# Performance work log

Hardware: AMD Instinct MI355X
Metric: run time of the kernel (lower is better)

## Reference

```python
import jax, jax.numpy as jnp
import numpy as np

N_NODES = 100000
N_EDGES = 1600000
D_IN, D_HID, N_CLS, N_LAYERS = 128, 256, 10, 3


def setup_inputs() -> dict:
    key = jax.random.key(0)
    ks = jax.random.split(key, 8)
    x = jax.random.normal(ks[0], (N_NODES, D_IN), dtype=jnp.float32)
    edge_index = jax.random.randint(ks[1], (2, N_EDGES), 0, N_NODES, dtype=jnp.int64)
    s = 0.05
    Wl = jax.random.normal(ks[2], (N_LAYERS, D_HID, D_IN), dtype=jnp.float32) * s
    Wr = jax.random.normal(ks[3], (N_LAYERS, D_HID, D_IN), dtype=jnp.float32) * s
    bias = jnp.zeros((N_LAYERS, D_HID), dtype=jnp.float32)
    W1 = jax.random.normal(ks[4], (D_HID, D_HID), dtype=jnp.float32) * s
    b1 = jnp.zeros((D_HID,), dtype=jnp.float32)
    W2 = jax.random.normal(ks[5], (N_CLS, D_HID), dtype=jnp.float32) * s
    b2 = jnp.zeros((N_CLS,), dtype=jnp.float32)
    return {"x": x, "edge_index": edge_index, "Wl": Wl, "Wr": Wr, "bias": bias,
            "W1": W1, "b1": b1, "W2": W2, "b2": b2}


def reference(x, edge_index, Wl, Wr, bias, W1, b1, W2, b2):
    n = x.shape[0]
    src, tgt = edge_index[0], edge_index[1]
    # mean aggregation of source-node features onto targets (SAGEConv aggr='mean')
    deg = jax.ops.segment_sum(jnp.ones(src.shape[0], x.dtype), tgt, num_segments=n)
    agg = jax.ops.segment_sum(x[src], tgt, num_segments=n)  # [N, D_in]
    agg = agg / jnp.clip(deg, 1.0)[:, None]
    # Every layer consumes the ORIGINAL x (per the source forward), so agg is shared.
    h = None
    for l in range(Wl.shape[0]):
        h = jax.nn.relu(agg @ Wl[l].T + x @ Wr[l].T + bias[l])  # [N, D_hid]
    # global_mean_pool over all nodes (single graph)
    pooled = jnp.mean(h, axis=0, keepdims=True)  # [1, D_hid]
    z = jax.nn.relu(pooled @ W1.T + b1)
    z = z @ W2.T + b2
    return jax.nn.log_softmax(z, axis=1)
```

## Files before the change

kernel.cpp:

```cpp
#include <hip/hip_runtime.h>
#include <hip/hip_bf16.h>

#define D_IN  128
#define D_HID 256
#define CBITS 9
#define CSIZE 512
#define EPB   8192
#define CCAP  10240
#define GT_CAP 2048

typedef __bf16 bf16x8 __attribute__((ext_vector_type(8)));
typedef float  f32x4  __attribute__((ext_vector_type(4)));
typedef float  f32x2  __attribute__((ext_vector_type(2)));

__device__ __forceinline__ unsigned short f2bf(float f) {
    unsigned u = __float_as_uint(f);
    u += 0x7FFFu + ((u >> 16) & 1u);
    return (unsigned short)(u >> 16);
}
__device__ __forceinline__ uint2 pack4(float4 v) {
    unsigned lo = (unsigned)f2bf(v.x) | ((unsigned)f2bf(v.y) << 16);
    unsigned hi = (unsigned)f2bf(v.z) | ((unsigned)f2bf(v.w) << 16);
    return make_uint2(lo, hi);
}
__device__ __forceinline__ unsigned packfp8(float4 v) {
    int u = __builtin_amdgcn_cvt_pk_fp8_f32(v.x, v.y, 0, false);
    u = __builtin_amdgcn_cvt_pk_fp8_f32(v.z, v.w, u, true);
    return (unsigned)u;
}
__device__ __forceinline__ void g2lds16(const void* g, void* l) {
    __builtin_amdgcn_global_load_lds(
        (const __attribute__((address_space(1))) unsigned int*)g,
        (__attribute__((address_space(3))) unsigned int*)l, 16, 0, 0);
}

__global__ __launch_bounds__(256)
void prep(const float* __restrict__ x, unsigned short* __restrict__ xb,
          unsigned char* __restrict__ x8,
          const float* __restrict__ Wr2, const float* __restrict__ Wl2,
          unsigned short* __restrict__ Bsw,
          int* __restrict__ gcur, float* __restrict__ pooled_pad,
          long n16, int NXB, int NCB) {
    const int bid = blockIdx.x;
    const int tid = threadIdx.x;
    if (bid < NXB) {
        const long t = (long)bid * 256 + tid;
        if (t >= n16) return;
        const float4* x4 = (const float4*)x;
        float4 v0 = x4[t * 4], v1 = x4[t * 4 + 1], v2 = x4[t * 4 + 2], v3 = x4[t * 4 + 3];
        uint2 p0 = pack4(v0), p1 = pack4(v1), p2 = pack4(v2), p3 = pack4(v3);
        ((uint4*)xb)[t * 2]     = make_uint4(p0.x, p0.y, p1.x, p1.y);
        ((uint4*)xb)[t * 2 + 1] = make_uint4(p2.x, p2.y, p3.x, p3.y);
        ((uint4*)x8)[t] = make_uint4(packfp8(v0), packfp8(v1), packfp8(v2), packfp8(v3));
    } else if (bid < NXB + 32) {
        const int t_idx = (bid - NXB) * 256 + tid;
        const int lane = t_idx & 63;
        const int rest = t_idx >> 6;
        const int tt   = rest & 3;
        const int wn2  = (rest >> 2) & 3;
        const int kk   = rest >> 4;
        const int j = wn2 * 64 + tt * 16 + (lane & 15);
        const int k = kk * 32 + (lane >> 4) * 8;
        const float* src = (k < 128) ? &Wr2[j * 128 + k] : &Wl2[j * 128 + (k - 128)];
        float4 v0 = *(const float4*)src;
        float4 v1 = *(const float4*)(src + 4);
        uint2 p0 = pack4(v0), p1 = pack4(v1);
        *(uint4*)&Bsw[(long)t_idx * 8] = make_uint4(p0.x, p0.y, p1.x, p1.y);
    } else {
        for (int i = tid; i < NCB * 16; i += 256) gcur[i] = 0;
        for (int i = tid; i < 256 * 16; i += 256) pooled_pad[i] = 0.f;
    }
}

__global__ __launch_bounds__(256)
void coarse_bin(const void* __restrict__ ei, int* __restrict__ gcur,
                unsigned* __restrict__ segc, int E, int NCB) {
    __shared__ int cnt[256];
    __shared__ int basel[256];
    __shared__ int s_is64;
    const int tid = threadIdx.x;
    const long e0 = (long)blockIdx.x * EPB;
    const int ecnt = (int)min((long)EPB, (long)E - e0);

    if (tid < 64) {
        const int v = ((const int*)ei)[2 * tid + 1];
        const unsigned long long b = __ballot(v != 0);
        if (tid == 0) s_is64 = (b == 0ull);
    }
    for (int i = tid; i < NCB; i += 256) cnt[i] = 0;
    __syncthreads();
    const int is64 = s_is64;

    for (int j = tid; j < ecnt; j += 256) {
        int t = is64 ? (int)((const long long*)ei)[E + e0 + j]
                     : ((const int*)ei)[E + e0 + j];
        atomicAdd(&cnt[t >> CBITS], 1);
    }
    __syncthreads();

    for (int c = tid; c < NCB; c += 256) {
        const int n = cnt[c];
        const int na = (n + 15) & ~15;
        int b = 0;
        if (na > 0) b = atomicAdd(&gcur[c * 16], na);
        basel[c] = b;
        cnt[c] = 0;
        unsigned* sp = segc + (long)c * CCAP;
        for (int i = n; i < na; ++i)
            if (b + i < CCAP) sp[b + i] = 0xFFFFFFFFu;
    }
    __syncthreads();

    for (int j = tid; j < ecnt; j += 256) {
        int s, t;
        if (is64) { const long long* p = (const long long*)ei; s = (int)p[e0 + j]; t = (int)p[E + e0 + j]; }
        else      { const int* p = (const int*)ei;             s = p[e0 + j];      t = p[E + e0 + j]; }
        const int c = t >> CBITS;
        const int r = atomicAdd(&cnt[c], 1);
        const int pos = basel[c] + r;
        if (pos < CCAP)
            segc[(long)c * CCAP + pos] = ((unsigned)s << CBITS) | (unsigned)(t & (CSIZE - 1));
    }
}

__global__ __launch_bounds__(1024)
void refine(const int* __restrict__ gcur, const unsigned* __restrict__ segc,
            unsigned* __restrict__ gorder, int2* __restrict__ rowdeg, int M) {
    __shared__ unsigned order[CCAP];
    __shared__ int degh[CSIZE], scn[CSIZE], cur[CSIZE];
    const int tid = threadIdx.x;
    const int cb = blockIdx.x;
    const int nbase = cb << CBITS;
    const int nn = min(CSIZE, M - nbase);
    const int len = min(gcur[cb * 16], CCAP);
    const unsigned* sp = segc + (long)cb * CCAP;

    if (tid < CSIZE) degh[tid] = 0;
    __syncthreads();
    for (int i = tid; i < len; i += 1024) {
        const unsigned e = sp[i];
        if (e != 0xFFFFFFFFu) atomicAdd(&degh[e & (CSIZE - 1)], 1);
    }
    __syncthreads();
    if (tid < CSIZE) scn[tid] = degh[tid];
    __syncthreads();
    for (int off = 1; off < CSIZE; off <<= 1) {
        int v = 0;
        if (tid >= off && tid < CSIZE) v = scn[tid - off];
        __syncthreads();
        if (tid < CSIZE) scn[tid] += v;
        __syncthreads();
    }
    if (tid < CSIZE) cur[tid] = scn[tid] - degh[tid];
    __syncthreads();
    for (int i = tid; i < len; i += 1024) {
        const unsigned e = sp[i];
        if (e != 0xFFFFFFFFu) {
            const int r = atomicAdd(&cur[e & (CSIZE - 1)], 1);
            order[r] = (e >> CBITS) << 7;
        }
    }
    __syncthreads();
    const int total = scn[CSIZE - 1];
    unsigned* gp = gorder + (long)cb * CCAP;
    for (int i = tid; i < total; i += 1024) gp[i] = order[i];
    if (tid < nn)
        rowdeg[nbase + tid] = make_int2(cb * CCAP + (scn[tid] - degh[tid]), degh[tid]);
}

__global__ __launch_bounds__(512)
void gather_tile(const unsigned char* __restrict__ x8, const unsigned* __restrict__ gorder,
                 const int2* __restrict__ rowdeg, unsigned short* __restrict__ aggb, int M) {
    __shared__ unsigned ordl[GT_CAP];
    __shared__ int s_start, s_total;
    const int tid = threadIdx.x;
    const int first = blockIdx.x * 64;
    const int nn = min(64, M - first);

    if (tid == 0) {
        int2 r0 = rowdeg[first];
        int2 rl = rowdeg[first + nn - 1];
        s_start = r0.x;
        s_total = min(rl.x + rl.y - r0.x, GT_CAP);
    }
    __syncthreads();
    const int st = s_start, tot = s_total;
    for (int i = tid; i < tot; i += 512) ordl[i] = gorder[st + i];
    __syncthreads();

    const int wave = tid >> 6;
    const int lane = tid & 63;
    const int c2   = lane & 15;
    const int sub  = lane >> 4;
    const unsigned cb = (unsigned)c2 * 8;

    for (int nl = wave; nl < nn; nl += 8) {
        const int node = first + nl;
        const int2 rd = rowdeg[node];
        const int beg = rd.x - st;
        const int deg = min(rd.y, tot - beg);
        f32x2 a0 = {0.f, 0.f}, a1 = {0.f, 0.f}, a2 = {0.f, 0.f}, a3 = {0.f, 0.f};
        int i = 0;
        const int nf = deg & ~7;
        for (; i < nf; i += 8) {
            uint2 v0 = *(const uint2*)(x8 + (ordl[beg + i + sub] + cb));
            uint2 v1 = *(const uint2*)(x8 + (ordl[beg + i + 4 + sub] + cb));
            a0 += __builtin_amdgcn_cvt_pk_f32_fp8(v0.x, false);
            a1 += __builtin_amdgcn_cvt_pk_f32_fp8(v0.x, true);
            a2 += __builtin_amdgcn_cvt_pk_f32_fp8(v0.y, false);
            a3 += __builtin_amdgcn_cvt_pk_f32_fp8(v0.y, true);
            a0 += __builtin_amdgcn_cvt_pk_f32_fp8(v1.x, false);
            a1 += __builtin_amdgcn_cvt_pk_f32_fp8(v1.x, true);
            a2 += __builtin_amdgcn_cvt_pk_f32_fp8(v1.y, false);
            a3 += __builtin_amdgcn_cvt_pk_f32_fp8(v1.y, true);
        }
        if (i < deg) {
            uint2 v0 = (i + sub < deg)
                     ? *(const uint2*)(x8 + (ordl[beg + i + sub] + cb)) : make_uint2(0, 0);
            uint2 v1 = (i + 4 + sub < deg)
                     ? *(const uint2*)(x8 + (ordl[beg + i + 4 + sub] + cb)) : make_uint2(0, 0);
            a0 += __builtin_amdgcn_cvt_pk_f32_fp8(v0.x, false);
            a1 += __builtin_amdgcn_cvt_pk_f32_fp8(v0.x, true);
            a2 += __builtin_amdgcn_cvt_pk_f32_fp8(v0.y, false);
            a3 += __builtin_amdgcn_cvt_pk_f32_fp8(v0.y, true);
            a0 += __builtin_amdgcn_cvt_pk_f32_fp8(v1.x, false);
            a1 += __builtin_amdgcn_cvt_pk_f32_fp8(v1.x, true);
            a2 += __builtin_amdgcn_cvt_pk_f32_fp8(v1.y, false);
            a3 += __builtin_amdgcn_cvt_pk_f32_fp8(v1.y, true);
        }
        a0.x += __shfl_xor(a0.x, 16); a0.x += __shfl_xor(a0.x, 32);
        a0.y += __shfl_xor(a0.y, 16); a0.y += __shfl_xor(a0.y, 32);
        a1.x += __shfl_xor(a1.x, 16); a1.x += __shfl_xor(a1.x, 32);
        a1.y += __shfl_xor(a1.y, 16); a1.y += __shfl_xor(a1.y, 32);
        a2.x += __shfl_xor(a2.x, 16); a2.x += __shfl_xor(a2.x, 32);
        a2.y += __shfl_xor(a2.y, 16); a2.y += __shfl_xor(a2.y, 32);
        a3.x += __shfl_xor(a3.x, 16); a3.x += __shfl_xor(a3.x, 32);
        a3.y += __shfl_xor(a3.y, 16); a3.y += __shfl_xor(a3.y, 32);
        if (sub == 0) {
            const float rdiv = 1.0f / fmaxf((float)rd.y, 1.0f);
            unsigned w0 = (unsigned)f2bf(a0.x * rdiv) | ((unsigned)f2bf(a0.y * rdiv) << 16);
            unsigned w1 = (unsigned)f2bf(a1.x * rdiv) | ((unsigned)f2bf(a1.y * rdiv) << 16);
            unsigned w2 = (unsigned)f2bf(a2.x * rdiv) | ((unsigned)f2bf(a2.y * rdiv) << 16);
            unsigned w3 = (unsigned)f2bf(a3.x * rdiv) | ((unsigned)f2bf(a3.y * rdiv) << 16);
            *(uint4*)(aggb + (long)node * 128 + c2 * 8) = make_uint4(w0, w1, w2, w3);
        }
    }
}

__global__ __launch_bounds__(256, 2)
void gemm_pool(const unsigned short* __restrict__ xb, const unsigned short* __restrict__ aggb,
               const unsigned short* __restrict__ Bsw, const float* __restrict__ bias2,
               float* __restrict__ pooled_pad, int M, int NT) {
    __shared__ unsigned short As[4 * 32 * 256];
    const int tid  = threadIdx.x;
    const int lane = tid & 63;
    const int wn2  = tid >> 6;
    const int lrow = lane & 15;
    const int quad = lane >> 4;
    const int bid  = blockIdx.x;
    const int GRID = gridDim.x;
    const int nt   = (NT - bid + GRID - 1) / GRID;
    if (nt <= 0) return;

    uint4 bb[8][4];
    #pragma unroll
    for (int kk = 0; kk < 8; ++kk)
        #pragma unroll
        for (int t = 0; t < 4; ++t)
            bb[kk][t] = *(const uint4*)&Bsw[((((long)kk * 4 + wn2) * 4 + t) * 64 + lane) * 8];
    float bv[4];
    #pragma unroll
    for (int t = 0; t < 4; ++t) bv[t] = bias2[wn2 * 64 + t * 16 + lrow];

    const int cl = tid & 31;
    const int rw = tid >> 5;
    const int cs = cl ^ rw;
    const unsigned short* sbase = (cs < 16) ? (xb + (long)cs * 8)
                                            : (aggb + (long)(cs - 16) * 8);
    char* lbase = (char*)As + rw * 512 + cl * 16;

    auto STAGE = [&](int p) {
        const long trow = ((long)bid + (long)p * GRID) * 32;
        char* ld = lbase + (p & 3) * 16384;
        #pragma unroll
        for (int s = 0; s < 4; ++s)
            g2lds16(sbase + (trow + s * 8 + rw) * 128, ld + s * 4096);
    };

    #pragma unroll
    for (int p = 0; p < 3; ++p) if (p < nt) STAGE(p);

    float ps[4] = {0.f, 0.f, 0.f, 0.f};

    for (int p = 0; p < nt; ++p) {
        const int rem = nt - 1 - p;
        if (rem >= 2)      asm volatile("s_waitcnt vmcnt(8)" ::: "memory");
        else if (rem == 1) asm volatile("s_waitcnt vmcnt(4)" ::: "memory");
        else               asm volatile("s_waitcnt vmcnt(0)" ::: "memory");
        __builtin_amdgcn_s_barrier();
        if (p + 3 < nt) STAGE(p + 3);

        const char* Ab = (const char*)As + (p & 3) * 16384;
        f32x4 acc[2][4] = {};
        #pragma unroll
        for (int kk = 0; kk < 8; ++kk) {
            uint4 aC[2];
            #pragma unroll
            for (int i = 0; i < 2; ++i) {
                const int r = i * 16 + lrow;
                aC[i] = *(const uint4*)(Ab + r * 512 + (((kk * 4 + quad) ^ (lrow & 7)) * 16));
            }
            #pragma unroll
            for (int i = 0; i < 2; ++i)
                #pragma unroll
                for (int t = 0; t < 4; ++t)
                    acc[i][t] = __builtin_amdgcn_mfma_f32_16x16x32_bf16(
                        *(bf16x8*)&aC[i], *(bf16x8*)&bb[kk][t], acc[i][t], 0, 0, 0);
        }

        const long trow = ((long)bid + (long)p * GRID) * 32;
        #pragma unroll
        for (int t = 0; t < 4; ++t) {
            float s = 0.f;
            #pragma unroll
            for (int i = 0; i < 2; ++i) {
                const long rbase = trow + i * 16 + quad * 4;
                #pragma unroll
                for (int r = 0; r < 4; ++r) {
                    float h = fmaxf(acc[i][t][r] + bv[t], 0.f);
                    if (rbase + r < M) s += h;
                }
            }
            ps[t] += s;
        }
    }

    #pragma unroll
    for (int t = 0; t < 4; ++t) {
        ps[t] += __shfl_xor(ps[t], 16);
        ps[t] += __shfl_xor(ps[t], 32);
        if (quad == 0)
            atomicAdd(&pooled_pad[(wn2 * 64 + t * 16 + lrow) * 16], ps[t]);
    }
}

__global__ __launch_bounds__(256)
void head_kernel(const float* __restrict__ pooled_pad,
                 const float* __restrict__ W1, const float* __restrict__ b1,
                 const float* __restrict__ W2, const float* __restrict__ b2,
                 float* __restrict__ out, float invM) {
    __shared__ float pooled_s[256];
    __shared__ float z1_s[256];
    __shared__ float z2_s[10];
    const int j = threadIdx.x;

    pooled_s[j] = pooled_pad[j * 16] * invM;
    __syncthreads();

    const float4* w4 = (const float4*)(W1 + (long)j * 256);
    float sx = 0.f, sy = 0.f, sz = 0.f, sw = 0.f;
    #pragma unroll 8
    for (int k = 0; k < 64; ++k) {
        float4 w = w4[k];
        float4 p = *(const float4*)&pooled_s[k * 4];
        sx += w.x * p.x; sy += w.y * p.y; sz += w.z * p.z; sw += w.w * p.w;
    }
    z1_s[j] = fmaxf(b1[j] + sx + sy + sz + sw, 0.f);
    __syncthreads();

    if (j < 160) {
        const int c = j >> 4, q = j & 15;
        float s = 0.f;
        for (int k = q; k < 256; k += 16) s += W2[c * 256 + k] * z1_s[k];
        #pragma unroll
        for (int off = 8; off >= 1; off >>= 1) s += __shfl_down(s, off, 16);
        if (q == 0) z2_s[c] = s + b2[c];
    }
    __syncthreads();

    if (j == 0) {
        float mx = z2_s[0];
        for (int c = 1; c < 10; ++c) mx = fmaxf(mx, z2_s[c]);
        float se = 0.f;
        for (int c = 0; c < 10; ++c) se += expf(z2_s[c] - mx);
        const float ls = logf(se);
        for (int c = 0; c < 10; ++c) out[c] = z2_s[c] - mx - ls;
    }
}

extern "C" void kernel_launch(void* const* d_in, const int* in_sizes, int n_in,
                              void* d_out, int out_size, void* d_ws, size_t ws_size,
                              hipStream_t stream) {
    const float* x    = (const float*)d_in[0];
    const void*  ei   = d_in[1];
    const float* Wl   = (const float*)d_in[2];
    const float* Wr   = (const float*)d_in[3];
    const float* bias = (const float*)d_in[4];
    const float* W1   = (const float*)d_in[5];
    const float* b1   = (const float*)d_in[6];
    const float* W2   = (const float*)d_in[7];
    const float* b2   = (const float*)d_in[8];
    float* out = (float*)d_out;

    const int M = in_sizes[0] / D_IN;
    const int E = in_sizes[1] / 2;
    const int L = in_sizes[4] / D_HID;
    const int NMB = (M + 127) / 128;
    const long Mpad = (long)NMB * 128;
    const int NCB = (M + CSIZE - 1) / CSIZE;
    const int NB1 = (E + EPB - 1) / EPB;
    const int NGT = (M + 63) / 64;
    const int NT  = (M + 31) / 32;
    const int NG  = (NT < 512) ? NT : 512;

    const float* Wl2   = Wl + (long)(L - 1) * D_HID * D_IN;
    const float* Wr2   = Wr + (long)(L - 1) * D_HID * D_IN;
    const float* bias2 = bias + (long)(L - 1) * D_HID;

    unsigned short* xb   = (unsigned short*)d_ws;
    unsigned short* aggb = xb + Mpad * D_IN;
    unsigned char*  x8   = (unsigned char*)(aggb + Mpad * D_IN);
    unsigned short* Bsw  = (unsigned short*)(x8 + Mpad * D_IN);
    float* pooled_pad    = (float*)(Bsw + 256 * 256);
    int*      gcur       = (int*)(pooled_pad + 256 * 16);
    unsigned* segc       = (unsigned*)(gcur + (long)NCB * 16);
    unsigned* gorder     = segc + (long)NCB * CCAP;
    int2*     rowdeg     = (int2*)(gorder + (long)NCB * CCAP);

    const long n16 = (long)M * 8;
    const int NXB = (int)((n16 + 255) / 256);

    prep<<<NXB + 32 + 1, 256, 0, stream>>>(x, xb, x8, Wr2, Wl2, Bsw, gcur, pooled_pad,
                                           n16, NXB, NCB);
    coarse_bin<<<NB1, 256, 0, stream>>>(ei, gcur, segc, E, NCB);
    refine<<<NCB, 1024, 0, stream>>>(gcur, segc, gorder, rowdeg, M);
    gather_tile<<<NGT, 512, 0, stream>>>(x8, gorder, rowdeg, aggb, M);

    gemm_pool<<<NG, 256, 0, stream>>>(xb, aggb, Bsw, bias2, pooled_pad, M, NT);

    head_kernel<<<1, 256, 0, stream>>>(pooled_pad, W1, b1, W2, b2, out, 1.0f / (float)M);
}
```

Baseline: 238.8 us.

## Fuse refine and gather into one kernel with smaller coarse bins

Merges the per-bin sort (refine) and the fp8 neighbor gather into a single kernel. The sorted order now stays in LDS instead of going through gorder/rowdeg in global memory, and one kernel launch is dropped. Bins shrink from 512 to 128 nodes (capacity 4096) so the order array fits in shared memory. The gather now assigns one node to each 16-lane group instead of a whole wave per node, which removes the cross-lane shuffle reduction but gives each lane a serial, less parallel edge loop. Coarse_bin must now track 4x more bins in shared memory and atomics.

```diff
diff --git a/kernel.cpp b/kernel.cpp
--- a/kernel.cpp
+++ b/kernel.cpp
@@ -3,11 +3,10 @@
 
 #define D_IN  128
 #define D_HID 256
-#define CBITS 9
-#define CSIZE 512
+#define CBITS 7
+#define CSIZE 128
 #define EPB   8192
-#define CCAP  10240
-#define GT_CAP 2048
+#define CCAP  4096
 
 typedef __bf16 bf16x8 __attribute__((ext_vector_type(8)));
 typedef float  f32x4  __attribute__((ext_vector_type(4)));
@@ -32,6 +31,12 @@
     __builtin_amdgcn_global_load_lds(
         (const __attribute__((address_space(1))) unsigned int*)g,
         (__attribute__((address_space(3))) unsigned int*)l, 16, 0, 0);
+}
+__device__ __forceinline__ void acc8(f32x2& a0, f32x2& a1, f32x2& a2, f32x2& a3, uint2 v) {
+    a0 += __builtin_amdgcn_cvt_pk_f32_fp8(v.x, false);
+    a1 += __builtin_amdgcn_cvt_pk_f32_fp8(v.x, true);
+    a2 += __builtin_amdgcn_cvt_pk_f32_fp8(v.y, false);
+    a3 += __builtin_amdgcn_cvt_pk_f32_fp8(v.y, true);
 }
 
 __global__ __launch_bounds__(256)
@@ -75,8 +80,8 @@
 __global__ __launch_bounds__(256)
 void coarse_bin(const void* __restrict__ ei, int* __restrict__ gcur,
                 unsigned* __restrict__ segc, int E, int NCB) {
-    __shared__ int cnt[256];
-    __shared__ int basel[256];
+    __shared__ int cnt[1024];
+    __shared__ int basel[1024];
     __shared__ int s_is64;
     const int tid = threadIdx.x;
     const long e0 = (long)blockIdx.x * EPB;
@@ -123,9 +128,10 @@
     }
 }
 
-__global__ __launch_bounds__(1024)
-void refine(const int* __restrict__ gcur, const unsigned* __restrict__ segc,
-            unsigned* __restrict__ gorder, int2* __restrict__ rowdeg, int M) {
+__global__ __launch_bounds__(512)
+void refine_gather(const int* __restrict__ gcur, const unsigned* __restrict__ segc,
+                   const unsigned char* __restrict__ x8,
+                   unsigned short* __restrict__ aggb, int M) {
     __shared__ unsigned order[CCAP];
     __shared__ int degh[CSIZE], scn[CSIZE], cur[CSIZE];
     const int tid = threadIdx.x;
@@ -137,7 +143,7 @@
 
     if (tid < CSIZE) degh[tid] = 0;
     __syncthreads();
-    for (int i = tid; i < len; i += 1024) {
+    for (int i = tid; i < len; i += 512) {
         const unsigned e = sp[i];
         if (e != 0xFFFFFFFFu) atomicAdd(&degh[e & (CSIZE - 1)], 1);
     }
@@ -153,96 +159,47 @@
     }
     if (tid < CSIZE) cur[tid] = scn[tid] - degh[tid];
     __syncthreads();
-    for (int i = tid; i < len; i += 1024) {
+    for (int i = tid; i < len; i += 512) {
         const unsigned e = sp[i];
         if (e != 0xFFFFFFFFu) {
             const int r = atomicAdd(&cur[e & (CSIZE - 1)], 1);
-            order[r] = (e >> CBITS) << 7;
-        }
-    }
-    __syncthreads();
-    const int total = scn[CSIZE - 1];
-    unsigned* gp = gorder + (long)cb * CCAP;
-    for (int i = tid; i < total; i += 1024) gp[i] = order[i];
-    if (tid < nn)
-        rowdeg[nbase + tid] = make_int2(cb * CCAP + (scn[tid] - degh[tid]), degh[tid]);
-}
-
-__global__ __launch_bounds__(512)
-void gather_tile(const unsigned char* __restrict__ x8, const unsigned* __restrict__ gorder,
-                 const int2* __restrict__ rowdeg, unsigned short* __restrict__ aggb, int M) {
-    __shared__ unsigned ordl[GT_CAP];
-    __shared__ int s_start, s_total;
-    const int tid = threadIdx.x;
-    const int first = blockIdx.x * 64;
-    const int nn = min(64, M - first);
-
-    if (tid == 0) {
-        int2 r0 = rowdeg[first];
-        int2 rl = rowdeg[first + nn - 1];
-        s_start = r0.x;
-        s_total = min(rl.x + rl.y - r0.x, GT_CAP);
-    }
-    __syncthreads();
-    const int st = s_start, tot = s_total;
-    for (int i = tid; i < tot; i += 512) ordl[i] = gorder[st + i];
-    __syncthreads();
-
+            order[r] = e & ~(unsigned)(CSIZE - 1);
+        }
+    }
+    __syncthreads();
+
+    const int lane = tid & 63;
     const int wave = tid >> 6;
-    const int lane = tid & 63;
+    const int ns   = lane >> 4;
     const int c2   = lane & 15;
-    const int sub  = lane >> 4;
-    const unsigned cb = (unsigned)c2 * 8;
-
-    for (int nl = wave; nl < nn; nl += 8) {
-        const int node = first + nl;
-        const int2 rd = rowdeg[node];
-        const int beg = rd.x - st;
-        const int deg = min(rd.y, tot - beg);
+    const unsigned chb = (unsigned)c2 * 8;
+
+    for (int base = wave * 4; base < nn; base += 32) {
+        const int nl = base + ns;
+        int deg = 0, beg = 0;
+        if (nl < nn) { deg = degh[nl]; beg = scn[nl] - deg; }
         f32x2 a0 = {0.f, 0.f}, a1 = {0.f, 0.f}, a2 = {0.f, 0.f}, a3 = {0.f, 0.f};
         int i = 0;
-        const int nf = deg & ~7;
-        for (; i < nf; i += 8) {
-            uint2 v0 = *(const uint2*)(x8 + (ordl[beg + i + sub] + cb));
-            uint2 v1 = *(const uint2*)(x8 + (ordl[beg + i + 4 + sub] + cb));
-            a0 += __builtin_amdgcn_cvt_pk_f32_fp8(v0.x, false);
-            a1 += __builtin_amdgcn_cvt_pk_f32_fp8(v0.x, true);
-            a2 += __builtin_amdgcn_cvt_pk_f32_fp8(v0.y, false);
-            a3 += __builtin_amdgcn_cvt_pk_f32_fp8(v0.y, true);
-            a0 += __builtin_amdgcn_cvt_pk_f32_fp8(v1.x, false);
-            a1 += __builtin_amdgcn_cvt_pk_f32_fp8(v1.x, true);
-            a2 += __builtin_amdgcn_cvt_pk_f32_fp8(v1.y, false);
-            a3 += __builtin_amdgcn_cvt_pk_f32_fp8(v1.y, true);
+        for (; i + 2 <= deg; i += 2) {
+            const unsigned o0 = order[beg + i];
+            const unsigned o1 = order[beg + i + 1];
+            uint2 v0 = *(const uint2*)(x8 + (o0 + chb));
+            uint2 v1 = *(const uint2*)(x8 + (o1 + chb));
+            acc8(a0, a1, a2, a3, v0);
+            acc8(a0, a1, a2, a3, v1);
         }
         if (i < deg) {
-            uint2 v0 = (i + sub < deg)
-                     ? *(const uint2*)(x8 + (ordl[beg + i + sub] + cb)) : make_uint2(0, 0);
-            uint2 v1 = (i + 4 + sub < deg)
-                     ? *(const uint2*)(x8 + (ordl[beg + i + 4 + sub] + cb)) : make_uint2(0, 0);
-            a0 += __builtin_amdgcn_cvt_pk_f32_fp8(v0.x, false);
-            a1 += __builtin_amdgcn_cvt_pk_f32_fp8(v0.x, true);
-            a2 += __builtin_amdgcn_cvt_pk_f32_fp8(v0.y, false);
-            a3 += __builtin_amdgcn_cvt_pk_f32_fp8(v0.y, true);
-            a0 += __builtin_amdgcn_cvt_pk_f32_fp8(v1.x, false);
-            a1 += __builtin_amdgcn_cvt_pk_f32_fp8(v1.x, true);
-            a2 += __builtin_amdgcn_cvt_pk_f32_fp8(v1.y, false);
-            a3 += __builtin_amdgcn_cvt_pk_f32_fp8(v1.y, true);
-        }
-        a0.x += __shfl_xor(a0.x, 16); a0.x += __shfl_xor(a0.x, 32);
-        a0.y += __shfl_xor(a0.y, 16); a0.y += __shfl_xor(a0.y, 32);
-        a1.x += __shfl_xor(a1.x, 16); a1.x += __shfl_xor(a1.x, 32);
-        a1.y += __shfl_xor(a1.y, 16); a1.y += __shfl_xor(a1.y, 32);
-        a2.x += __shfl_xor(a2.x, 16); a2.x += __shfl_xor(a2.x, 32);
-        a2.y += __shfl_xor(a2.y, 16); a2.y += __shfl_xor(a2.y, 32);
-        a3.x += __shfl_xor(a3.x, 16); a3.x += __shfl_xor(a3.x, 32);
-        a3.y += __shfl_xor(a3.y, 16); a3.y += __shfl_xor(a3.y, 32);
-        if (sub == 0) {
-            const float rdiv = 1.0f / fmaxf((float)rd.y, 1.0f);
+            const unsigned o0 = order[beg + i];
+            uint2 v0 = *(const uint2*)(x8 + (o0 + chb));
+            acc8(a0, a1, a2, a3, v0);
+        }
+        if (nl < nn) {
+            const float rdiv = 1.0f / fmaxf((float)deg, 1.0f);
             unsigned w0 = (unsigned)f2bf(a0.x * rdiv) | ((unsigned)f2bf(a0.y * rdiv) << 16);
             unsigned w1 = (unsigned)f2bf(a1.x * rdiv) | ((unsigned)f2bf(a1.y * rdiv) << 16);
             unsigned w2 = (unsigned)f2bf(a2.x * rdiv) | ((unsigned)f2bf(a2.y * rdiv) << 16);
             unsigned w3 = (unsigned)f2bf(a3.x * rdiv) | ((unsigned)f2bf(a3.y * rdiv) << 16);
-            *(uint4*)(aggb + (long)node * 128 + c2 * 8) = make_uint4(w0, w1, w2, w3);
+            *(uint4*)(aggb + (long)(nbase + nl) * 128 + c2 * 8) = make_uint4(w0, w1, w2, w3);
         }
     }
 }
@@ -409,7 +366,6 @@
     const long Mpad = (long)NMB * 128;
     const int NCB = (M + CSIZE - 1) / CSIZE;
     const int NB1 = (E + EPB - 1) / EPB;
-    const int NGT = (M + 63) / 64;
     const int NT  = (M + 31) / 32;
     const int NG  = (NT < 512) ? NT : 512;
 
@@ -424,8 +380,6 @@
     float* pooled_pad    = (float*)(Bsw + 256 * 256);
     int*      gcur       = (int*)(pooled_pad + 256 * 16);
     unsigned* segc       = (unsigned*)(gcur + (long)NCB * 16);
-    unsigned* gorder     = segc + (long)NCB * CCAP;
-    int2*     rowdeg     = (int2*)(gorder + (long)NCB * CCAP);
 
     const long n16 = (long)M * 8;
     const int NXB = (int)((n16 + 255) / 256);
@@ -433,8 +387,7 @@
     prep<<<NXB + 32 + 1, 256, 0, stream>>>(x, xb, x8, Wr2, Wl2, Bsw, gcur, pooled_pad,
                                            n16, NXB, NCB);
     coarse_bin<<<NB1, 256, 0, stream>>>(ei, gcur, segc, E, NCB);
-    refine<<<NCB, 1024, 0, stream>>>(gcur, segc, gorder, rowdeg, M);
-    gather_tile<<<NGT, 512, 0, stream>>>(x8, gorder, rowdeg, aggb, M);
+    refine_gather<<<NCB, 512, 0, stream>>>(gcur, segc, x8, aggb, M);
 
     gemm_pool<<<NG, 256, 0, stream>>>(xb, aggb, Bsw, bias2, pooled_pad, M, NT);
 
```

Result: no change. 235.2 us (-1.5%).
